# Kernel tuning notes

Measured on AMD Instinct MI355X. Metric: run time of the kernel, lower is better.

## Reference

```python
import jax, jax.numpy as jnp
import numpy as np

HEADS = 16
D_MODEL = 1024
IMG_MODEL = 512
D_K = D_MODEL // HEADS


def setup_inputs() -> dict:
    key = jax.random.key(0)
    ks = jax.random.split(key, 12)
    B, LQ, LKV = 8, 2048, 1024
    s_dm = 1.0 / np.sqrt(D_MODEL)
    s_im = 1.0 / np.sqrt(IMG_MODEL)
    return {
        "q": jax.random.normal(ks[0], (B, LQ, D_MODEL), jnp.float32),
        "k": jax.random.normal(ks[1], (B, LKV, IMG_MODEL), jnp.float32),
        "v": jax.random.normal(ks[2], (B, LKV, IMG_MODEL), jnp.float32),
        "Wq": jax.random.normal(ks[3], (D_MODEL, D_MODEL), jnp.float32) * s_dm,
        "bq": jnp.zeros((D_MODEL,), jnp.float32),
        "Wk": jax.random.normal(ks[4], (IMG_MODEL, D_MODEL), jnp.float32) * s_im,
        "bk": jnp.zeros((D_MODEL,), jnp.float32),
        "Wv": jax.random.normal(ks[5], (IMG_MODEL, D_MODEL), jnp.float32) * s_im,
        "bv": jnp.zeros((D_MODEL,), jnp.float32),
        "Wo": jax.random.normal(ks[6], (D_MODEL, D_MODEL), jnp.float32) * s_dm,
        "bo": jnp.zeros((D_MODEL,), jnp.float32),
    }


def reference(q, k, v, Wq, bq, Wk, bk, Wv, bv, Wo, bo):
    B, LQ, _ = q.shape
    LKV = k.shape[1]
    # projections -> [B, H, L, d_k]
    qh = (q @ Wq + bq).reshape(B, LQ, HEADS, D_K).transpose(0, 2, 1, 3)
    kh = (k @ Wk + bk).reshape(B, LKV, HEADS, D_K).transpose(0, 2, 1, 3)
    vh = (v @ Wv + bv).reshape(B, LKV, HEADS, D_K).transpose(0, 2, 1, 3)
    scale = 1.0 / np.sqrt(D_K)
    scores = jnp.einsum("bhqd,bhkd->bhqk", qh, kh) * scale  # [B,H,LQ,LKV]
    attn = jax.nn.softmax(scores, axis=-1)  # dropout = identity at eval
    out = jnp.einsum("bhqk,bhkd->bhqd", attn, vh)  # [B,H,LQ,d_k]
    concat = out.transpose(0, 2, 1, 3).reshape(B, LQ, D_MODEL)
    return concat @ Wo + bo
```

## Files before the change

### kernel.cpp

```cpp
#include <hip/hip_runtime.h>

typedef __bf16 bf16;
typedef __bf16 bf16x8 __attribute__((ext_vector_type(8)));
typedef __bf16 bf16x4 __attribute__((ext_vector_type(4)));
typedef float f32x4 __attribute__((ext_vector_type(4)));

constexpr int BB   = 8;
constexpr int LQ   = 2048;
constexpr int LKV  = 1024;
constexpr int DM   = 1024;
constexpr int DIMG = 512;
constexpr int H    = 16;
constexpr int DK   = 64;

__device__ inline void async16(const bf16* g, bf16* l) {
  __builtin_amdgcn_global_load_lds((const __attribute__((address_space(1))) void*)g,
                                   (__attribute__((address_space(3))) void*)l, 16, 0, 0);
}
__device__ inline float fexp2(float x) { return __builtin_amdgcn_exp2f(x); }

__global__ __launch_bounds__(256) void cvt_all(const float* __restrict__ q,
                                               const float* __restrict__ k,
                                               const float* __restrict__ v,
                                               bf16* __restrict__ qo,
                                               bf16* __restrict__ ko,
                                               bf16* __restrict__ vo,
                                               int nq4, int nk4) {
  int i = blockIdx.x * 256 + threadIdx.x;
  const float* in;
  bf16* out;
  int idx;
  if (i < nq4) { in = q; out = qo; idx = i; }
  else if (i < nq4 + nk4) { in = k; out = ko; idx = i - nq4; }
  else if (i < nq4 + 2 * nk4) { in = v; out = vo; idx = i - nq4 - nk4; }
  else return;
  const float4 f = ((const float4*)in)[idx];
  bf16x4 o;
  o[0] = (bf16)f.x; o[1] = (bf16)f.y; o[2] = (bf16)f.z; o[3] = (bf16)f.w;
  ((bf16x4*)out)[idx] = o;
}

__global__ __launch_bounds__(256) void transpose_all(const float* __restrict__ Wq,
                                                     const float* __restrict__ Wk,
                                                     const float* __restrict__ Wv,
                                                     const float* __restrict__ Wo,
                                                     bf16* __restrict__ WqT,
                                                     bf16* __restrict__ WkT,
                                                     bf16* __restrict__ WvT,
                                                     bf16* __restrict__ WoT) {
  const int z = blockIdx.z;
  const float* W;
  bf16* WT;
  int K;
  if (z == 0) { W = Wq; WT = WqT; K = DM; }
  else if (z == 1) { W = Wk; WT = WkT; K = DIMG; }
  else if (z == 2) { W = Wv; WT = WvT; K = DIMG; }
  else { W = Wo; WT = WoT; K = DM; }
  const int N = DM;
  if (blockIdx.x * 64 >= K) return;

  __shared__ float tile[64][65];
  const int k0 = blockIdx.x * 64, n0 = blockIdx.y * 64;
  const int tx = threadIdx.x & 63, tg = threadIdx.x >> 6;
#pragma unroll
  for (int i = 0; i < 16; ++i) {
    int row = tg * 16 + i;
    tile[row][tx] = W[(size_t)(k0 + row) * N + n0 + tx];
  }
  __syncthreads();
#pragma unroll
  for (int i = 0; i < 16; ++i) {
    int nrow = tg * 16 + i;
    WT[(size_t)(n0 + nrow) * K + k0 + tx] = (bf16)tile[tx][nrow];
  }
}

template <typename OutT, bool VT_OUT>
__global__ __launch_bounds__(256) void gemm_bt(const bf16* __restrict__ A,
                                               const bf16* __restrict__ Bt,
                                               const float* __restrict__ bias,
                                               OutT* __restrict__ C,
                                               int M, int N, int K, float oscale) {
  __shared__ __align__(16) bf16 As[128 * 32];
  __shared__ __align__(16) bf16 Bs[128 * 32];

  const int tid = threadIdx.x, lane = tid & 63, wave = tid >> 6;
  const int bm = blockIdx.x, bn = blockIdx.y;
  const int wm = (wave & 1) * 64, wn = (wave >> 1) * 64;
  const int fm = lane & 15, quad = lane >> 4, fk8 = quad * 8;

  f32x4 acc[4][4];
#pragma unroll
  for (int i = 0; i < 4; ++i)
#pragma unroll
    for (int j = 0; j < 4; ++j) {
      f32x4 z = {0.f, 0.f, 0.f, 0.f};
      acc[i][j] = z;
    }

  const int srow = lane >> 2, scol = (lane & 3) * 8;
  const bf16* Ab = A + (size_t)(bm * 128) * K;
  const bf16* Bb = Bt + (size_t)(bn * 128) * K;
  const bf16* ag0 = Ab + (size_t)(wave * 16 + srow) * K + scol;
  const bf16* ag1 = ag0 + (size_t)64 * K;
  const bf16* bg0 = Bb + (size_t)(wave * 16 + srow) * K + scol;
  const bf16* bg1 = bg0 + (size_t)64 * K;
  bf16* la0 = &As[(wave * 16) * 32];
  bf16* la1 = &As[(64 + wave * 16) * 32];
  bf16* lb0 = &Bs[(wave * 16) * 32];
  bf16* lb1 = &Bs[(64 + wave * 16) * 32];

  for (int k0 = 0; k0 < K; k0 += 32) {
    async16(ag0 + k0, la0);
    async16(ag1 + k0, la1);
    async16(bg0 + k0, lb0);
    async16(bg1 + k0, lb1);
    __syncthreads();
    bf16x8 af[4], bfr[4];
#pragma unroll
    for (int i = 0; i < 4; ++i)
      af[i] = *(const bf16x8*)&As[(wm + i * 16 + fm) * 32 + fk8];
#pragma unroll
    for (int j = 0; j < 4; ++j)
      bfr[j] = *(const bf16x8*)&Bs[(wn + j * 16 + fm) * 32 + fk8];
#pragma unroll
    for (int i = 0; i < 4; ++i)
#pragma unroll
      for (int j = 0; j < 4; ++j)
        acc[i][j] = __builtin_amdgcn_mfma_f32_16x16x32_bf16(af[i], bfr[j], acc[i][j], 0, 0, 0);
    __syncthreads();
  }

#pragma unroll
  for (int j = 0; j < 4; ++j) {
    const int col = bn * 128 + wn + j * 16 + fm;
    const float bv = bias[col];
    if constexpr (VT_OUT) {
      const int h = col >> 6, dk = col & 63;
#pragma unroll
      for (int i = 0; i < 4; ++i) {
        const int row = bm * 128 + wm + i * 16 + quad * 4;
        const int b = row >> 10, t = row & 1023;
        bf16x4 o;
#pragma unroll
        for (int r = 0; r < 4; ++r) o[r] = (bf16)((acc[i][j][r] + bv) * oscale);
        *(bf16x4*)&C[(((size_t)(b * H + h) * DK + dk) << 10) + t] = o;
      }
    } else {
#pragma unroll
      for (int i = 0; i < 4; ++i) {
#pragma unroll
        for (int r = 0; r < 4; ++r) {
          const int row = bm * 128 + wm + i * 16 + quad * 4 + r;
          C[(size_t)row * N + col] = (OutT)((acc[i][j][r] + bv) * oscale);
        }
      }
    }
  }
}

__global__ __launch_bounds__(256, 3) void attn_kernel(const bf16* __restrict__ qh,
                                                      const bf16* __restrict__ kh,
                                                      const bf16* __restrict__ vt,
                                                      bf16* __restrict__ out) {
  constexpr int NT = LKV / 64;
  __shared__ __align__(16) bf16 Ks[2][64 * 64];
  __shared__ __align__(16) bf16 Vs[2][64 * 64];
  __shared__ __align__(16) bf16 Ps[4][32 * 64];

  const int tid = threadIdx.x, lane = tid & 63, w = tid >> 6;
  const int fm = lane & 15, quad = lane >> 4;
  const int qt = blockIdx.x, h = blockIdx.y, b = blockIdx.z;
  const int q0 = qt * 128;

  const bf16* qbase = qh + ((size_t)(b * LQ) + q0 + w * 32) * DM + h * DK;
  const bf16* kbase = kh + (size_t)(b * LKV) * DM + h * DK;
  const bf16* vbase = vt + (size_t)(b * H + h) * DK * LKV;

  bf16x8 qf[2][2];
#pragma unroll
  for (int i = 0; i < 2; ++i)
#pragma unroll
    for (int kg = 0; kg < 2; ++kg)
      qf[i][kg] = *(const bf16x8*)&qbase[(size_t)(i * 16 + fm) * DM + kg * 32 + quad * 8];

  const int srow = lane >> 3, sslot = lane & 7;
  const int fs = fm & 7;

  auto stage = [&](int t, int bf) {
#pragma unroll
    for (int c = 0; c < 2; ++c) {
      const int r0 = w * 16 + c * 8;
      const int row = r0 + srow;
      const int gs = (sslot ^ (row & 7)) << 3;
      async16(kbase + (size_t)(t * 64 + row) * DM + gs, &Ks[bf][r0 * 64]);
      async16(vbase + (size_t)row * LKV + t * 64 + gs, &Vs[bf][r0 * 64]);
    }
  };

  stage(0, 0);
  stage(1, 1);

  float row_m[2] = {-1e30f, -1e30f}, row_l[2] = {0.f, 0.f};
  f32x4 o_acc[2][4];
#pragma unroll
  for (int i = 0; i < 2; ++i)
#pragma unroll
    for (int jd = 0; jd < 4; ++jd) {
      f32x4 z = {0.f, 0.f, 0.f, 0.f};
      o_acc[i][jd] = z;
    }

  bf16* Pw = Ps[w];

#pragma unroll 2
  for (int t = 0; t < NT; ++t) {
    asm volatile("s_waitcnt vmcnt(4)" ::: "memory");
    __builtin_amdgcn_s_barrier();
    __builtin_amdgcn_sched_barrier(0);
    const bf16* Kb = Ks[t & 1];
    const bf16* Vb = Vs[t & 1];

    f32x4 s[4][2];
#pragma unroll
    for (int m = 0; m < 4; ++m)
#pragma unroll
      for (int i = 0; i < 2; ++i) {
        f32x4 z = {0.f, 0.f, 0.f, 0.f};
        s[m][i] = z;
      }
    __builtin_amdgcn_s_setprio(1);
#pragma unroll
    for (int kg = 0; kg < 2; ++kg)
#pragma unroll
      for (int m = 0; m < 4; ++m) {
        const bf16x8 kf =
            *(const bf16x8*)&Kb[(m * 16 + fm) * 64 + (((kg * 4 + quad) ^ fs) << 3)];
#pragma unroll
        for (int i = 0; i < 2; ++i)
          s[m][i] = __builtin_amdgcn_mfma_f32_16x16x32_bf16(kf, qf[i][kg], s[m][i], 0, 0, 0);
      }
    __builtin_amdgcn_s_setprio(0);

#pragma unroll
    for (int i = 0; i < 2; ++i) {
      float pm[4];
#pragma unroll
      for (int m = 0; m < 4; ++m)
        pm[m] = fmaxf(fmaxf(s[m][i][0], s[m][i][1]), fmaxf(s[m][i][2], s[m][i][3]));
      float mt = fmaxf(fmaxf(pm[0], pm[1]), fmaxf(pm[2], pm[3]));
      mt = fmaxf(mt, __shfl_xor(mt, 16));
      mt = fmaxf(mt, __shfl_xor(mt, 32));
      float alpha = 1.f;
      if (!__all(mt <= row_m[i] + 8.0f)) {
        const float nm = fmaxf(row_m[i], mt);
        alpha = fexp2(row_m[i] - nm);
        row_m[i] = nm;
#pragma unroll
        for (int r = 0; r < 4; ++r) {
          const float a_o = __shfl(alpha, quad * 4 + r);
#pragma unroll
          for (int jd = 0; jd < 4; ++jd) o_acc[i][jd][r] *= a_o;
        }
      }
      const float mi = row_m[i];
      float pp[4];
#pragma unroll
      for (int m = 0; m < 4; ++m) {
#pragma unroll
        for (int r = 0; r < 4; ++r) s[m][i][r] = fexp2(s[m][i][r] - mi);
        pp[m] = (s[m][i][0] + s[m][i][1]) + (s[m][i][2] + s[m][i][3]);
      }
      float ps = (pp[0] + pp[1]) + (pp[2] + pp[3]);
      ps += __shfl_xor(ps, 16);
      ps += __shfl_xor(ps, 32);
      row_l[i] = row_l[i] * alpha + ps;
    }

#pragma unroll
    for (int i = 0; i < 2; ++i)
#pragma unroll
      for (int m = 0; m < 4; ++m) {
        bf16x4 p4;
#pragma unroll
        for (int r = 0; r < 4; ++r) p4[r] = (bf16)s[m][i][r];
        *(bf16x4*)&Pw[(i * 16 + fm) * 64 + (((m * 2 + (quad >> 1)) ^ fs) << 3) +
                      ((quad & 1) << 2)] = p4;
      }

    __builtin_amdgcn_s_setprio(1);
#pragma unroll
    for (int kg = 0; kg < 2; ++kg) {
      bf16x8 pf[2];
#pragma unroll
      for (int i = 0; i < 2; ++i)
        pf[i] = *(const bf16x8*)&Pw[(i * 16 + fm) * 64 + (((kg * 4 + quad) ^ fs) << 3)];
#pragma unroll
      for (int jd = 0; jd < 4; ++jd) {
        const bf16x8 vfr =
            *(const bf16x8*)&Vb[(jd * 16 + fm) * 64 + (((kg * 4 + quad) ^ fs) << 3)];
#pragma unroll
        for (int i = 0; i < 2; ++i)
          o_acc[i][jd] = __builtin_amdgcn_mfma_f32_16x16x32_bf16(pf[i], vfr, o_acc[i][jd], 0, 0, 0);
      }
    }
    __builtin_amdgcn_s_setprio(0);

    __builtin_amdgcn_sched_barrier(0);
    __builtin_amdgcn_s_barrier();
    __builtin_amdgcn_sched_barrier(0);
    if (t < NT - 1) {
      const int tn = (t + 2 < NT) ? (t + 2) : (NT - 1);
      stage(tn, t & 1);
    }
  }
  asm volatile("s_waitcnt vmcnt(0)" ::: "memory");

  const float linv0 = 1.0f / row_l[0], linv1 = 1.0f / row_l[1];
  bf16* obase = out + ((size_t)(b * LQ) + q0 + w * 32) * DM + h * DK;
#pragma unroll
  for (int i = 0; i < 2; ++i) {
    const float li = i ? linv1 : linv0;
#pragma unroll
    for (int r = 0; r < 4; ++r) {
      const float lo = __shfl(li, quad * 4 + r);
#pragma unroll
      for (int jd = 0; jd < 4; ++jd)
        obase[(size_t)(i * 16 + quad * 4 + r) * DM + jd * 16 + fm] =
            (bf16)(o_acc[i][jd][r] * lo);
    }
  }
}

extern "C" void kernel_launch(void* const* d_in, const int* in_sizes, int n_in,
                              void* d_out, int out_size, void* d_ws, size_t ws_size,
                              hipStream_t stream) {
  const float* q  = (const float*)d_in[0];
  const float* k  = (const float*)d_in[1];
  const float* v  = (const float*)d_in[2];
  const float* Wq = (const float*)d_in[3];
  const float* bq = (const float*)d_in[4];
  const float* Wk = (const float*)d_in[5];
  const float* bk = (const float*)d_in[6];
  const float* Wv = (const float*)d_in[7];
  const float* bv = (const float*)d_in[8];
  const float* Wo = (const float*)d_in[9];
  const float* bo = (const float*)d_in[10];
  float* out = (float*)d_out;

  char* ws = (char*)d_ws;
  size_t off = 0;
  auto alloc = [&](size_t bytes) -> void* {
    void* p = ws + off;
    off += (bytes + 255) & ~(size_t)255;
    return p;
  };

  const size_t nq = (size_t)BB * LQ * DM;
  const size_t nk = (size_t)BB * LKV * DIMG;
  const size_t nkh = (size_t)BB * LKV * DM;

  bf16* qbf = (bf16*)alloc(nq * 2);
  bf16* kbf = (bf16*)alloc(nk * 2);
  bf16* vbf = (bf16*)alloc(nk * 2);
  bf16* WqT = (bf16*)alloc((size_t)DM * DM * 2);
  bf16* WkT = (bf16*)alloc((size_t)DM * DIMG * 2);
  bf16* WvT = (bf16*)alloc((size_t)DM * DIMG * 2);
  bf16* WoT = (bf16*)alloc((size_t)DM * DM * 2);
  bf16* qh  = (bf16*)alloc(nq * 2);
  bf16* kh  = (bf16*)alloc(nkh * 2);
  bf16* Vt  = (bf16*)alloc(nkh * 2);
  bf16* attn_out = qbf;

  const int nq4 = (int)(nq / 4), nk4 = (int)(nk / 4);
  cvt_all<<<(nq4 + 2 * nk4 + 255) / 256, 256, 0, stream>>>(q, k, v, qbf, kbf, vbf, nq4, nk4);

  transpose_all<<<dim3(DM / 64, DM / 64, 4), 256, 0, stream>>>(Wq, Wk, Wv, Wo, WqT, WkT, WvT, WoT);

  const float QSCALE = 0.125f * 1.44269504f;
  gemm_bt<bf16, false><<<dim3(BB * LQ / 128, DM / 128), 256, 0, stream>>>(
      qbf, WqT, bq, qh, BB * LQ, DM, DM, QSCALE);
  gemm_bt<bf16, false><<<dim3(BB * LKV / 128, DM / 128), 256, 0, stream>>>(
      kbf, WkT, bk, kh, BB * LKV, DM, DIMG, 1.0f);
  gemm_bt<bf16, true><<<dim3(BB * LKV / 128, DM / 128), 256, 0, stream>>>(
      vbf, WvT, bv, Vt, BB * LKV, DM, DIMG, 1.0f);

  attn_kernel<<<dim3(LQ / 128, H, BB), 256, 0, stream>>>(qh, kh, Vt, attn_out);

  gemm_bt<float, false><<<dim3(BB * LQ / 128, DM / 128), 256, 0, stream>>>(
      attn_out, WoT, bo, out, BB * LQ, DM, DM, 1.0f);
}
```

Baseline: 423.5 us.

## Double-buffer GEMM tiles, fuse K/V projections, remap blocks per XCD, widen attention blocks

The GEMM body now double-buffers its LDS tiles, so the next K-slice loads while the current one feeds the MFMAs. The grid is flattened with an XCD-aware block swizzle to improve L2 locality. The K and V projections are merged into one launch. The attention kernel moves to 512-thread blocks covering 256 query rows, so K/V tiles staged in LDS are shared by eight waves instead of four, with the wait count adjusted to match. This costs more LDS per block, and the single barrier per GEMM iteration with double buffering may race when a buffer is overwritten while still being read.

```diff
diff --git a/kernel.cpp b/kernel.cpp
--- a/kernel.cpp
+++ b/kernel.cpp
@@ -76,16 +76,13 @@
 }
 
 template <typename OutT, bool VT_OUT>
-__global__ __launch_bounds__(256) void gemm_bt(const bf16* __restrict__ A,
-                                               const bf16* __restrict__ Bt,
-                                               const float* __restrict__ bias,
-                                               OutT* __restrict__ C,
-                                               int M, int N, int K, float oscale) {
-  __shared__ __align__(16) bf16 As[128 * 32];
-  __shared__ __align__(16) bf16 Bs[128 * 32];
-
+__device__ __forceinline__ void gemm_body(const bf16* __restrict__ A,
+                                          const bf16* __restrict__ Bt,
+                                          const float* __restrict__ bias,
+                                          OutT* __restrict__ C,
+                                          int N, int K, float oscale, int bm, int bn,
+                                          bf16* As, bf16* Bs) {
   const int tid = threadIdx.x, lane = tid & 63, wave = tid >> 6;
-  const int bm = blockIdx.x, bn = blockIdx.y;
   const int wm = (wave & 1) * 64, wn = (wave >> 1) * 64;
   const int fm = lane & 15, quad = lane >> 4, fk8 = quad * 8;
 
@@ -99,30 +96,39 @@
     }
 
   const int srow = lane >> 2, scol = (lane & 3) * 8;
-  const bf16* Ab = A + (size_t)(bm * 128) * K;
-  const bf16* Bb = Bt + (size_t)(bn * 128) * K;
-  const bf16* ag0 = Ab + (size_t)(wave * 16 + srow) * K + scol;
+  const bf16* ag0 = A + (size_t)(bm * 128 + wave * 16 + srow) * K + scol;
   const bf16* ag1 = ag0 + (size_t)64 * K;
-  const bf16* bg0 = Bb + (size_t)(wave * 16 + srow) * K + scol;
+  const bf16* bg0 = Bt + (size_t)(bn * 128 + wave * 16 + srow) * K + scol;
   const bf16* bg1 = bg0 + (size_t)64 * K;
-  bf16* la0 = &As[(wave * 16) * 32];
-  bf16* la1 = &As[(64 + wave * 16) * 32];
-  bf16* lb0 = &Bs[(wave * 16) * 32];
-  bf16* lb1 = &Bs[(64 + wave * 16) * 32];
-
-  for (int k0 = 0; k0 < K; k0 += 32) {
-    async16(ag0 + k0, la0);
-    async16(ag1 + k0, la1);
-    async16(bg0 + k0, lb0);
-    async16(bg1 + k0, lb1);
-    __syncthreads();
+  bf16* la0 = As + (wave * 16) * 32;
+  bf16* la1 = As + (64 + wave * 16) * 32;
+  bf16* lb0 = Bs + (wave * 16) * 32;
+  bf16* lb1 = Bs + (64 + wave * 16) * 32;
+
+  const int KT = K >> 5;
+  async16(ag0, la0);
+  async16(ag1, la1);
+  async16(bg0, lb0);
+  async16(bg1, lb1);
+  __syncthreads();
+
+  for (int t = 0; t < KT; ++t) {
+    const int cur = (t & 1) * (128 * 32);
+    if (t + 1 < KT) {
+      const int nxt = ((t + 1) & 1) * (128 * 32);
+      const int k0 = (t + 1) * 32;
+      async16(ag0 + k0, la0 + nxt);
+      async16(ag1 + k0, la1 + nxt);
+      async16(bg0 + k0, lb0 + nxt);
+      async16(bg1 + k0, lb1 + nxt);
+    }
     bf16x8 af[4], bfr[4];
 #pragma unroll
     for (int i = 0; i < 4; ++i)
-      af[i] = *(const bf16x8*)&As[(wm + i * 16 + fm) * 32 + fk8];
+      af[i] = *(const bf16x8*)&As[cur + (wm + i * 16 + fm) * 32 + fk8];
 #pragma unroll
     for (int j = 0; j < 4; ++j)
-      bfr[j] = *(const bf16x8*)&Bs[(wn + j * 16 + fm) * 32 + fk8];
+      bfr[j] = *(const bf16x8*)&Bs[cur + (wn + j * 16 + fm) * 32 + fk8];
 #pragma unroll
     for (int i = 0; i < 4; ++i)
 #pragma unroll
@@ -159,19 +165,54 @@
   }
 }
 
-__global__ __launch_bounds__(256, 3) void attn_kernel(const bf16* __restrict__ qh,
+template <typename OutT>
+__global__ __launch_bounds__(256) void gemm_one(const bf16* __restrict__ A,
+                                                const bf16* __restrict__ Bt,
+                                                const float* __restrict__ bias,
+                                                OutT* __restrict__ C,
+                                                int N, int K, float oscale) {
+  __shared__ __align__(16) bf16 As[2 * 128 * 32];
+  __shared__ __align__(16) bf16 Bs[2 * 128 * 32];
+  const int cpx = gridDim.x >> 3;
+  const int wg = ((int)blockIdx.x & 7) * cpx + ((int)blockIdx.x >> 3);
+  const int nbn = N >> 7;
+  gemm_body<OutT, false>(A, Bt, bias, C, N, K, oscale, wg / nbn, wg % nbn, As, Bs);
+}
+
+__global__ __launch_bounds__(256) void gemm_kv(const bf16* __restrict__ kbf,
+                                               const bf16* __restrict__ WkT,
+                                               const float* __restrict__ bk,
+                                               bf16* __restrict__ kh,
+                                               const bf16* __restrict__ vbf,
+                                               const bf16* __restrict__ WvT,
+                                               const float* __restrict__ bv,
+                                               bf16* __restrict__ Vt) {
+  __shared__ __align__(16) bf16 As[2 * 128 * 32];
+  __shared__ __align__(16) bf16 Bs[2 * 128 * 32];
+  const int cpx = gridDim.x >> 3;
+  const int wg = ((int)blockIdx.x & 7) * cpx + ((int)blockIdx.x >> 3);
+  const int bn = wg & 7;
+  const int rest = wg >> 3;
+  const int bm = rest & 63;
+  if (rest < 64)
+    gemm_body<bf16, false>(kbf, WkT, bk, kh, DM, DIMG, 1.0f, bm, bn, As, Bs);
+  else
+    gemm_body<bf16, true>(vbf, WvT, bv, Vt, DM, DIMG, 1.0f, bm, bn, As, Bs);
+}
+
+__global__ __launch_bounds__(512, 4) void attn_kernel(const bf16* __restrict__ qh,
                                                       const bf16* __restrict__ kh,
                                                       const bf16* __restrict__ vt,
                                                       bf16* __restrict__ out) {
   constexpr int NT = LKV / 64;
   __shared__ __align__(16) bf16 Ks[2][64 * 64];
   __shared__ __align__(16) bf16 Vs[2][64 * 64];
-  __shared__ __align__(16) bf16 Ps[4][32 * 64];
+  __shared__ __align__(16) bf16 Ps[8][32 * 64];
 
   const int tid = threadIdx.x, lane = tid & 63, w = tid >> 6;
   const int fm = lane & 15, quad = lane >> 4;
   const int qt = blockIdx.x, h = blockIdx.y, b = blockIdx.z;
-  const int q0 = qt * 128;
+  const int q0 = qt * 256;
 
   const bf16* qbase = qh + ((size_t)(b * LQ) + q0 + w * 32) * DM + h * DK;
   const bf16* kbase = kh + (size_t)(b * LKV) * DM + h * DK;
@@ -188,14 +229,11 @@
   const int fs = fm & 7;
 
   auto stage = [&](int t, int bf) {
-#pragma unroll
-    for (int c = 0; c < 2; ++c) {
-      const int r0 = w * 16 + c * 8;
-      const int row = r0 + srow;
-      const int gs = (sslot ^ (row & 7)) << 3;
-      async16(kbase + (size_t)(t * 64 + row) * DM + gs, &Ks[bf][r0 * 64]);
-      async16(vbase + (size_t)row * LKV + t * 64 + gs, &Vs[bf][r0 * 64]);
-    }
+    const int r0 = w * 8;
+    const int row = r0 + srow;
+    const int gs = (sslot ^ (row & 7)) << 3;
+    async16(kbase + (size_t)(t * 64 + row) * DM + gs, &Ks[bf][r0 * 64]);
+    async16(vbase + (size_t)row * LKV + t * 64 + gs, &Vs[bf][r0 * 64]);
   };
 
   stage(0, 0);
@@ -215,7 +253,7 @@
 
 #pragma unroll 2
   for (int t = 0; t < NT; ++t) {
-    asm volatile("s_waitcnt vmcnt(4)" ::: "memory");
+    asm volatile("s_waitcnt vmcnt(2)" ::: "memory");
     __builtin_amdgcn_s_barrier();
     __builtin_amdgcn_sched_barrier(0);
     const bf16* Kb = Ks[t & 1];
@@ -378,15 +416,13 @@
   transpose_all<<<dim3(DM / 64, DM / 64, 4), 256, 0, stream>>>(Wq, Wk, Wv, Wo, WqT, WkT, WvT, WoT);
 
   const float QSCALE = 0.125f * 1.44269504f;
-  gemm_bt<bf16, false><<<dim3(BB * LQ / 128, DM / 128), 256, 0, stream>>>(
-      qbf, WqT, bq, qh, BB * LQ, DM, DM, QSCALE);
-  gemm_bt<bf16, false><<<dim3(BB * LKV / 128, DM / 128), 256, 0, stream>>>(
-      kbf, WkT, bk, kh, BB * LKV, DM, DIMG, 1.0f);
-  gemm_bt<bf16, true><<<dim3(BB * LKV / 128, DM / 128), 256, 0, stream>>>(
-      vbf, WvT, bv, Vt, BB * LKV, DM, DIMG, 1.0f);
-
-  attn_kernel<<<dim3(LQ / 128, H, BB), 256, 0, stream>>>(qh, kh, Vt, attn_out);
-
-  gemm_bt<float, false><<<dim3(BB * LQ / 128, DM / 128), 256, 0, stream>>>(
-      attn_out, WoT, bo, out, BB * LQ, DM, DM, 1.0f);
-}
+  gemm_one<bf16><<<(BB * LQ / 128) * (DM / 128), 256, 0, stream>>>(
+      qbf, WqT, bq, qh, DM, DM, QSCALE);
+  gemm_kv<<<(BB * LKV / 128) * (DM / 128) * 2, 256, 0, stream>>>(
+      kbf, WkT, bk, kh, vbf, WvT, bv, Vt);
+
+  attn_kernel<<<dim3(LQ / 256, H, BB), 512, 0, stream>>>(qh, kh, Vt, attn_out);
+
+  gemm_one<float><<<(BB * LQ / 128) * (DM / 128), 256, 0, stream>>>(
+      attn_out, WoT, bo, out, BB * LQ == 0 ? DM : DM, DM, 1.0f);
+}
```

New measurement: 399.4 us. -5.7%, faster.
